# Optimization experiments

Hardware: AMD Instinct MI355X
Metric: run time of the kernel (lower is better)

Reference implementation:

```python
import jax, jax.numpy as jnp
import numpy as np

NUM_LOCAL = 4      # num_local_experts
E_TOTAL = 8        # local + unpopular experts
HIDDEN = 1024
FFN = 4 * HIDDEN
CAP = 2048         # tokens (capacity) per expert
D0 = 1             # leading dim of inputs / output_tensor


def setup_inputs() -> dict:
    key = jax.random.key(0)
    k_in, k_w0, k_w3 = jax.random.split(key, 3)
    inputs = jax.random.normal(k_in, (D0, E_TOTAL, CAP, HIDDEN), dtype=jnp.float32)
    # gating-activity indicator per expert; all-ones -> all unpopular experts active
    output_tensor = jnp.ones((D0, E_TOTAL), dtype=jnp.float32)
    # stacked per-expert MLP weights (torch Linear convention: [out, in])
    w0 = jax.random.normal(k_w0, (E_TOTAL, FFN, HIDDEN), dtype=jnp.float32) * 0.02
    w3 = jax.random.normal(k_w3, (E_TOTAL, HIDDEN, FFN), dtype=jnp.float32) * 0.02
    return {"output_tensor": output_tensor, "inputs": inputs, "w0": w0, "w3": w3}


def reference(output_tensor, inputs, w0, w3):
    # Grouped 2-layer MLP per expert: x @ w0^T -> GELU -> @ w3^T
    # b: D0, e: expert, c: capacity, d: hidden, f: ffn
    h = jnp.einsum('becd,efd->becf', inputs, w0)
    h = jax.nn.gelu(h, approximate=False)  # torch nn.GELU default = exact erf
    out = jnp.einsum('becf,edf->becd', h, w3)
    # unpopular experts with zero activity produce zeros (scatter-into-zeros combine)
    unpop_mask = jnp.sum(output_tensor[:, NUM_LOCAL:], axis=0) != 0  # [E_unpop]
    full_mask = jnp.concatenate(
        [jnp.ones((NUM_LOCAL,), dtype=bool), unpop_mask])  # locals always computed
    out = out * full_mask[None, :, None, None].astype(out.dtype)
    return out
```

## Files before the change

kernel.cpp:

```cpp
#include <hip/hip_runtime.h>
#include <math.h>

#define E_TOTAL 8
#define NUM_LOCAL 4
#define HIDDEN 1024
#define FFN 4096
#define CAP 2048

typedef unsigned short ushort_t;
typedef __attribute__((ext_vector_type(8))) short short8;
typedef __attribute__((ext_vector_type(4))) float f32x4;

__device__ __forceinline__ unsigned short f2bf(float f) {
  unsigned int u = __float_as_uint(f);
  u += 0x7FFFu + ((u >> 16) & 1u);
  return (unsigned short)(u >> 16);
}

__device__ __forceinline__ void gload_lds16(const void* g, void* l) {
  __builtin_amdgcn_global_load_lds(
      (const __attribute__((address_space(1))) void*)g,
      (__attribute__((address_space(3))) void*)l,
      16, 0, 0);
}

__global__ __launch_bounds__(256) void cvt_kernel(const float4* __restrict__ s,
                                                  ushort4* __restrict__ d) {
  const size_t i = (size_t)blockIdx.x * 256 + threadIdx.x;
  float4 v = s[i];
  d[i] = make_ushort4(f2bf(v.x), f2bf(v.y), f2bf(v.z), f2bf(v.w));
}

template <int M, int N, int K, bool GELU_OUT>
__global__ __launch_bounds__(256, 2) void gemm_nt(
    const ushort_t* __restrict__ A, const ushort_t* __restrict__ B,
    void* __restrict__ Cout, const float* __restrict__ ot, int d0) {
  __shared__ ushort_t lds_a[128 * 32];
  __shared__ ushort_t lds_b[128 * 32];

  const int e = blockIdx.z;
  const int bm = blockIdx.x * 128;
  const int bn = blockIdx.y * 128;
  const int t = threadIdx.x;
  const int wave = t >> 6, lane = t & 63;
  const int wr = wave >> 1, wc = wave & 1;
  const int quad = lane >> 4, l16 = lane & 15;
  const int sub = lane >> 2, qc = lane & 3;

  const ushort_t* Ag = A + (size_t)e * M * K + (size_t)bm * K;
  const ushort_t* Bg = B + (size_t)e * N * K + (size_t)bn * K;

  f32x4 acc[4][4];
#pragma unroll
  for (int i = 0; i < 4; ++i)
#pragma unroll
    for (int j = 0; j < 4; ++j) {
      f32x4 z = {0.f, 0.f, 0.f, 0.f};
      acc[i][j] = z;
    }

  for (int kb = 0; kb < K / 32; ++kb) {
    const ushort_t* Ak = Ag + kb * 32 + (size_t)sub * K + qc * 8;
    const ushort_t* Bk = Bg + kb * 32 + (size_t)sub * K + qc * 8;
#pragma unroll
    for (int r = 0; r < 2; ++r) {
      const int chunk = r * 4 + wave;
      gload_lds16(Ak + (size_t)chunk * 16 * K, &lds_a[chunk * 512]);
      gload_lds16(Bk + (size_t)chunk * 16 * K, &lds_b[chunk * 512]);
    }
    __syncthreads();

    short8 af[4], bf[4];
#pragma unroll
    for (int i = 0; i < 4; ++i) {
      af[i] = *(const short8*)&lds_a[(wr * 64 + i * 16 + l16) * 32 + quad * 8];
      bf[i] = *(const short8*)&lds_b[(wc * 64 + i * 16 + l16) * 32 + quad * 8];
    }
#pragma unroll
    for (int mi = 0; mi < 4; ++mi)
#pragma unroll
      for (int ni = 0; ni < 4; ++ni)
        acc[mi][ni] = __builtin_amdgcn_mfma_f32_16x16x32_bf16(
            af[mi], bf[ni], acc[mi][ni], 0, 0, 0);
    __syncthreads();
  }

  if (GELU_OUT) {
    ushort_t* C = (ushort_t*)Cout + (size_t)e * M * N +
                  (size_t)(bm + wr * 64) * N + (bn + wc * 64);
#pragma unroll
    for (int mi = 0; mi < 4; ++mi)
#pragma unroll
      for (int r = 0; r < 4; ++r) {
        const int row = mi * 16 + quad * 4 + r;
#pragma unroll
        for (int ni = 0; ni < 4; ++ni) {
          float v = acc[mi][ni][r];
          v = 0.5f * v * (1.f + erff(v * 0.70710678118654752f));
          C[(size_t)row * N + ni * 16 + l16] = f2bf(v);
        }
      }
  } else {
    float mask = 1.f;
    if (e >= NUM_LOCAL) {
      float s = 0.f;
      for (int b = 0; b < d0; ++b) s += ot[b * E_TOTAL + e];
      mask = (s != 0.f) ? 1.f : 0.f;
    }
    float* C = (float*)Cout + (size_t)e * M * N +
               (size_t)(bm + wr * 64) * N + (bn + wc * 64);
#pragma unroll
    for (int mi = 0; mi < 4; ++mi)
#pragma unroll
      for (int r = 0; r < 4; ++r) {
        const int row = mi * 16 + quad * 4 + r;
#pragma unroll
        for (int ni = 0; ni < 4; ++ni)
          C[(size_t)row * N + ni * 16 + l16] = acc[mi][ni][r] * mask;
      }
  }
}

extern "C" void kernel_launch(void* const* d_in, const int* in_sizes, int n_in,
                              void* d_out, int out_size, void* d_ws,
                              size_t ws_size, hipStream_t stream) {
  const float* ot = (const float*)d_in[0];
  const float* x  = (const float*)d_in[1];
  const float* w0 = (const float*)d_in[2];
  const float* w3 = (const float*)d_in[3];
  const int d0 = in_sizes[0] / E_TOTAL;

  char* ws = (char*)d_ws;
  ushort_t* xb  = (ushort_t*)ws;
  ushort_t* w0b = (ushort_t*)(ws + (size_t)32 * 1024 * 1024);
  ushort_t* w3b = (ushort_t*)ws;
  ushort_t* h   = (ushort_t*)(ws + (size_t)96 * 1024 * 1024);

  const int n4x = E_TOTAL * CAP * HIDDEN / 4;
  const int n4w = E_TOTAL * FFN * HIDDEN / 4;

  cvt_kernel<<<n4x / 256, 256, 0, stream>>>((const float4*)x, (ushort4*)xb);
  cvt_kernel<<<n4w / 256, 256, 0, stream>>>((const float4*)w0, (ushort4*)w0b);

  gemm_nt<CAP, FFN, HIDDEN, true>
      <<<dim3(CAP / 128, FFN / 128, E_TOTAL), 256, 0, stream>>>(
          xb, w0b, h, nullptr, d0);

  cvt_kernel<<<n4w / 256, 256, 0, stream>>>((const float4*)w3, (ushort4*)w3b);

  gemm_nt<CAP, HIDDEN, FFN, false>
      <<<dim3(CAP / 128, HIDDEN / 128, E_TOTAL), 256, 0, stream>>>(
          h, w3b, d_out, ot, d0);
}
```

Baseline: 702.0 us.

## Double GEMM K-tile to 64 with XOR-rotated LDS layout and wider conversion stores

Each GEMM main-loop iteration now loads a 64-wide K slice instead of 32. This halves the number of barrier pairs per tile and doubles the MFMA work between syncs. The LDS layout uses a per-row rotation of 16-byte chunks so fragment reads avoid bank conflicts. The fp32-to-bf16 conversion kernel now writes 16-byte vectors covering 8 elements per thread. LDS use per block doubles, which could affect occupancy at two blocks per CU.

```diff
diff --git a/kernel.cpp b/kernel.cpp
--- a/kernel.cpp
+++ b/kernel.cpp
@@ -9,6 +9,7 @@
 
 typedef unsigned short ushort_t;
 typedef __attribute__((ext_vector_type(8))) short short8;
+typedef __attribute__((ext_vector_type(8))) unsigned short u16x8;
 typedef __attribute__((ext_vector_type(4))) float f32x4;
 
 __device__ __forceinline__ unsigned short f2bf(float f) {
@@ -25,18 +26,21 @@
 }
 
 __global__ __launch_bounds__(256) void cvt_kernel(const float4* __restrict__ s,
-                                                  ushort4* __restrict__ d) {
+                                                  u16x8* __restrict__ d) {
   const size_t i = (size_t)blockIdx.x * 256 + threadIdx.x;
-  float4 v = s[i];
-  d[i] = make_ushort4(f2bf(v.x), f2bf(v.y), f2bf(v.z), f2bf(v.w));
+  float4 a = s[2 * i], b = s[2 * i + 1];
+  u16x8 o;
+  o[0] = f2bf(a.x); o[1] = f2bf(a.y); o[2] = f2bf(a.z); o[3] = f2bf(a.w);
+  o[4] = f2bf(b.x); o[5] = f2bf(b.y); o[6] = f2bf(b.z); o[7] = f2bf(b.w);
+  d[i] = o;
 }
 
 template <int M, int N, int K, bool GELU_OUT>
 __global__ __launch_bounds__(256, 2) void gemm_nt(
     const ushort_t* __restrict__ A, const ushort_t* __restrict__ B,
     void* __restrict__ Cout, const float* __restrict__ ot, int d0) {
-  __shared__ ushort_t lds_a[128 * 32];
-  __shared__ ushort_t lds_b[128 * 32];
+  __shared__ ushort_t lds_a[128 * 64];
+  __shared__ ushort_t lds_b[128 * 64];
 
   const int e = blockIdx.z;
   const int bm = blockIdx.x * 128;
@@ -45,10 +49,12 @@
   const int wave = t >> 6, lane = t & 63;
   const int wr = wave >> 1, wc = wave & 1;
   const int quad = lane >> 4, l16 = lane & 15;
-  const int sub = lane >> 2, qc = lane & 3;
+  const int r8 = lane >> 3;
+  const int s8 = lane & 7;
+  const int g8 = (s8 + r8) & 7;
 
-  const ushort_t* Ag = A + (size_t)e * M * K + (size_t)bm * K;
-  const ushort_t* Bg = B + (size_t)e * N * K + (size_t)bn * K;
+  const ushort_t* Ag = A + (size_t)e * M * K + (size_t)(bm + r8) * K + g8 * 8;
+  const ushort_t* Bg = B + (size_t)e * N * K + (size_t)(bn + r8) * K + g8 * 8;
 
   f32x4 acc[4][4];
 #pragma unroll
@@ -59,29 +65,34 @@
       acc[i][j] = z;
     }
 
-  for (int kb = 0; kb < K / 32; ++kb) {
-    const ushort_t* Ak = Ag + kb * 32 + (size_t)sub * K + qc * 8;
-    const ushort_t* Bk = Bg + kb * 32 + (size_t)sub * K + qc * 8;
+  for (int kb = 0; kb < K / 64; ++kb) {
+    const size_t ko = (size_t)kb * 64;
 #pragma unroll
-    for (int r = 0; r < 2; ++r) {
-      const int chunk = r * 4 + wave;
-      gload_lds16(Ak + (size_t)chunk * 16 * K, &lds_a[chunk * 512]);
-      gload_lds16(Bk + (size_t)chunk * 16 * K, &lds_b[chunk * 512]);
+    for (int j = 0; j < 4; ++j) {
+      const int R = (j * 4 + wave) * 8;
+      gload_lds16(Ag + ko + (size_t)R * K, &lds_a[R * 64]);
+      gload_lds16(Bg + ko + (size_t)R * K, &lds_b[R * 64]);
     }
     __syncthreads();
 
-    short8 af[4], bf[4];
 #pragma unroll
-    for (int i = 0; i < 4; ++i) {
-      af[i] = *(const short8*)&lds_a[(wr * 64 + i * 16 + l16) * 32 + quad * 8];
-      bf[i] = *(const short8*)&lds_b[(wc * 64 + i * 16 + l16) * 32 + quad * 8];
+    for (int ks = 0; ks < 2; ++ks) {
+      short8 af[4], bfr[4];
+      const int c = ks * 4 + quad;
+#pragma unroll
+      for (int i = 0; i < 4; ++i) {
+        const int ra = wr * 64 + i * 16 + l16;
+        const int rb = wc * 64 + i * 16 + l16;
+        af[i]  = *(const short8*)&lds_a[ra * 64 + ((c - ra) & 7) * 8];
+        bfr[i] = *(const short8*)&lds_b[rb * 64 + ((c - rb) & 7) * 8];
+      }
+#pragma unroll
+      for (int mi = 0; mi < 4; ++mi)
+#pragma unroll
+        for (int ni = 0; ni < 4; ++ni)
+          acc[mi][ni] = __builtin_amdgcn_mfma_f32_16x16x32_bf16(
+              af[mi], bfr[ni], acc[mi][ni], 0, 0, 0);
     }
-#pragma unroll
-    for (int mi = 0; mi < 4; ++mi)
-#pragma unroll
-      for (int ni = 0; ni < 4; ++ni)
-        acc[mi][ni] = __builtin_amdgcn_mfma_f32_16x16x32_bf16(
-            af[mi], bf[ni], acc[mi][ni], 0, 0, 0);
     __syncthreads();
   }
 
@@ -136,17 +147,17 @@
   ushort_t* w3b = (ushort_t*)ws;
   ushort_t* h   = (ushort_t*)(ws + (size_t)96 * 1024 * 1024);
 
-  const int n4x = E_TOTAL * CAP * HIDDEN / 4;
-  const int n4w = E_TOTAL * FFN * HIDDEN / 4;
+  const int nx = E_TOTAL * CAP * HIDDEN;
+  const int nw = E_TOTAL * FFN * HIDDEN;
 
-  cvt_kernel<<<n4x / 256, 256, 0, stream>>>((const float4*)x, (ushort4*)xb);
-  cvt_kernel<<<n4w / 256, 256, 0, stream>>>((const float4*)w0, (ushort4*)w0b);
+  cvt_kernel<<<nx / (256 * 8), 256, 0, stream>>>((const float4*)x, (u16x8*)xb);
+  cvt_kernel<<<nw / (256 * 8), 256, 0, stream>>>((const float4*)w0, (u16x8*)w0b);
 
   gemm_nt<CAP, FFN, HIDDEN, true>
       <<<dim3(CAP / 128, FFN / 128, E_TOTAL), 256, 0, stream>>>(
           xb, w0b, h, nullptr, d0);
 
-  cvt_kernel<<<n4w / 256, 256, 0, stream>>>((const float4*)w3, (ushort4*)w3b);
+  cvt_kernel<<<nw / (256 * 8), 256, 0, stream>>>((const float4*)w3, (u16x8*)w3b);
 
   gemm_nt<CAP, HIDDEN, FFN, false>
       <<<dim3(CAP / 128, HIDDEN / 128, E_TOTAL), 256, 0, stream>>>(
```

After: 677.0 us. -3.6%, faster.
